# Performance work log

Measured on AMD Instinct MI355X. Metric: run time of the kernel, lower is better.

The kernel has to match this reference:

```python
import jax, jax.numpy as jnp
import numpy as np

B, T, D = 4, 4096, 1024

def setup_inputs() -> dict:
    key = jax.random.key(0)
    kx, kq, kk, kv = jax.random.split(key, 4)
    return {
        "x": jax.random.normal(kx, (B, T, D), dtype=jnp.float32),
        "w_q": jax.random.normal(kq, (D, D), dtype=jnp.float32),
        "w_k": jax.random.normal(kk, (D, D), dtype=jnp.float32),
        "w_v": jax.random.normal(kv, (D, D), dtype=jnp.float32),
    }

def reference(x, w_q, w_k, w_v):
    # Projections: (B,T,D) @ (D,D) -> (B,T,D)
    q = jnp.einsum('btk,kd->btd', x, w_q)
    k = jnp.einsum('btk,kd->btd', x, w_k)
    v = jnp.einsum('btk,kd->btd', x, w_v)
    d = x.shape[-1]
    # Faithful to source: gamma = 1/sqrt(1/d) = sqrt(d) (multiplies, not divides)
    gamma = jnp.sqrt(jnp.asarray(d, dtype=x.dtype))
    a = jnp.einsum('bqd,bkd->bqk', q, k) * gamma  # (B,T,T), no softmax
    y = jnp.einsum('bqt,btd->bqd', a, v)          # (B,T,D)
    return y
```

## Files before the change

### kernel.cpp

```cpp
#include <hip/hip_runtime.h>
#include <hip/hip_bf16.h>


typedef __attribute__((ext_vector_type(8))) short bf16x8;
typedef __attribute__((ext_vector_type(4))) float f32x4;

__device__ __forceinline__ unsigned short bf16bits(float f) {
    union { __hip_bfloat16 b; unsigned short s; } r;
    r.b = __float2bfloat16(f);
    return r.s;
}

__device__ __forceinline__ void gload16(const void* g, void* l) {
    __builtin_amdgcn_global_load_lds((__attribute__((address_space(1))) void*)g,
                                     (__attribute__((address_space(3))) void*)l,
                                     16, 0, 0);
}

template<int TM, int TN, bool OUT_F32>
__global__ __launch_bounds__(256)
void gemm_nt(const __hip_bfloat16* __restrict__ Ap, const __hip_bfloat16* __restrict__ Bp,
             void* __restrict__ Cp, int N, int Kc, int ldA, int ldB,
             long sA, long sB, long sC, int nb, float scale)
{
    constexpr int FM = TM / 32;
    constexpr int FN = TN / 32;

    __shared__ __hip_bfloat16 At[TM][32];
    __shared__ __hip_bfloat16 Bt[TN][32];

    const int bz    = blockIdx.z;
    const int batch = bz % nb;
    const int kc    = bz / nb;

    int wg = blockIdx.y * gridDim.x + blockIdx.x;
    const int cpx = (int)(gridDim.x * gridDim.y) >> 3;
    wg = (wg & 7) * cpx + (wg >> 3);
    const int n0 = (wg % (int)gridDim.x) * TN;
    const int m0 = (wg / (int)gridDim.x) * TM;

    const int tid  = threadIdx.x;
    const int lane = tid & 63;
    const int wave = tid >> 6;
    const int wm = (wave & 1) * (TM / 2);
    const int wn = (wave >> 1) * (TN / 2);
    const int l16 = lane & 15;
    const int lq  = lane >> 4;

    const int aoff = wave * (TM * 8) + lane * 8;
    const int boff = wave * (TN * 8) + lane * 8;

    const __hip_bfloat16* Ab = Ap + (size_t)batch * sA + (size_t)kc * Kc;
    const __hip_bfloat16* Bb = Bp + (size_t)batch * sB + (size_t)kc * Kc;

    f32x4 acc[FM][FN];
    #pragma unroll
    for (int i = 0; i < FM; ++i)
        #pragma unroll
        for (int j = 0; j < FN; ++j)
            acc[i][j] = (f32x4){0.f, 0.f, 0.f, 0.f};

    for (int k0 = 0; k0 < Kc; k0 += 32) {
        #pragma unroll
        for (int i = 0; i < TM / 64; ++i) {
            const __hip_bfloat16* s =
                Ab + (size_t)(m0 + (aoff >> 5) + i * 16) * ldA + k0 + (aoff & 31);
            gload16(s, (__hip_bfloat16*)At + aoff + i * 512);
        }
        #pragma unroll
        for (int i = 0; i < TN / 64; ++i) {
            const __hip_bfloat16* s =
                Bb + (size_t)(n0 + (boff >> 5) + i * 16) * ldB + k0 + (boff & 31);
            gload16(s, (__hip_bfloat16*)Bt + boff + i * 512);
        }
        __syncthreads();

        bf16x8 av[FM], bv[FN];
        #pragma unroll
        for (int i = 0; i < FM; ++i)
            av[i] = *(const bf16x8*)&At[wm + i * 16 + l16][lq * 8];
        #pragma unroll
        for (int j = 0; j < FN; ++j)
            bv[j] = *(const bf16x8*)&Bt[wn + j * 16 + l16][lq * 8];
        #pragma unroll
        for (int i = 0; i < FM; ++i)
            #pragma unroll
            for (int j = 0; j < FN; ++j)
                acc[i][j] = __builtin_amdgcn_mfma_f32_16x16x32_bf16(av[i], bv[j], acc[i][j], 0, 0, 0);
        __syncthreads();
    }

    float* Cf = (float*)Cp;
    __hip_bfloat16* Ch = (__hip_bfloat16*)Cp;
    const size_t cb0 = (size_t)bz * sC;
    #pragma unroll
    for (int i = 0; i < FM; ++i) {
        #pragma unroll
        for (int j = 0; j < FN; ++j) {
            const int row0 = m0 + wm + i * 16 + lq * 4;
            const int col  = n0 + wn + j * 16 + l16;
            #pragma unroll
            for (int r = 0; r < 4; ++r) {
                float v = acc[i][j][r] * scale;
                size_t idx = cb0 + (size_t)(row0 + r) * N + col;
                if (OUT_F32) Cf[idx] = v;
                else         Ch[idx] = __float2bfloat16(v);
            }
        }
    }
}

__global__ __launch_bounds__(256)
void reduce_kchunks(const unsigned short* __restrict__ part,
                    unsigned short* __restrict__ out)
{
    const size_t l = ((size_t)blockIdx.x * 256 + threadIdx.x) * 8;
    const size_t DD4 = (size_t)4 << 20;
    union { unsigned short h[8]; uint4 u; } a, b, o;
    a.u = *(const uint4*)(part + l);
    b.u = *(const uint4*)(part + l + DD4);
    #pragma unroll
    for (int j = 0; j < 8; ++j) {
        union { float f; unsigned int u; } fa, fb;
        fa.u = (unsigned int)a.h[j] << 16;
        fb.u = (unsigned int)b.h[j] << 16;
        o.h[j] = bf16bits(fa.f + fb.f);
    }
    *(uint4*)(out + l) = o.u;
}

#define TP 64
__global__ __launch_bounds__(256)
void transpose_cast(const float* __restrict__ in, __hip_bfloat16* __restrict__ out,
                    __hip_bfloat16* __restrict__ straight, int nsb,
                    int R, int C, long inStride, long outStride)
{
    __shared__ __hip_bfloat16 t2[TP][TP + 4];
    const int b  = blockIdx.z;
    const int r0 = blockIdx.x * TP;
    const int c0 = blockIdx.y * TP;
    const float* inb = in + (size_t)b * inStride;
    __hip_bfloat16* outb = out + (size_t)b * outStride;
    __hip_bfloat16* stb  = straight + (size_t)b * inStride;
    const int t  = threadIdx.x;
    const int rr = t >> 4;
    const int c4 = (t & 15) * 4;
    #pragma unroll
    for (int p = 0; p < 4; ++p) {
        const int row = p * 16 + rr;
        float4 f = *(const float4*)&inb[(size_t)(r0 + row) * C + c0 + c4];
        union { __hip_bfloat16 h[4]; uint2 u; } s;
        s.h[0] = __float2bfloat16(f.x); s.h[1] = __float2bfloat16(f.y);
        s.h[2] = __float2bfloat16(f.z); s.h[3] = __float2bfloat16(f.w);
        t2[c4 + 0][row] = s.h[0];
        t2[c4 + 1][row] = s.h[1];
        t2[c4 + 2][row] = s.h[2];
        t2[c4 + 3][row] = s.h[3];
        if (b < nsb)
            *(uint2*)&stb[(size_t)(r0 + row) * C + c0 + c4] = s.u;
    }
    __syncthreads();
    #pragma unroll
    for (int p = 0; p < 4; ++p) {
        const int crow = p * 16 + rr;
        union { __hip_bfloat16 h[4]; uint2 u; } o;
        #pragma unroll
        for (int j = 0; j < 4; ++j) o.h[j] = t2[crow][c4 + j];
        *(uint2*)&outb[(size_t)(c0 + crow) * R + r0 + c4] = o.u;
    }
}

__global__ __launch_bounds__(256)
void cast_f32_bf16(const float* __restrict__ in, __hip_bfloat16* __restrict__ out, int n)
{
    const int i = (blockIdx.x * 256 + threadIdx.x) << 2;
    if (i >= n) return;
    float4 f = *(const float4*)(in + i);
    union { __hip_bfloat16 h[4]; uint2 u; } t;
    t.h[0] = __float2bfloat16(f.x); t.h[1] = __float2bfloat16(f.y);
    t.h[2] = __float2bfloat16(f.z); t.h[3] = __float2bfloat16(f.w);
    *(uint2*)(out + i) = t.u;
}

extern "C" void kernel_launch(void* const* d_in, const int* in_sizes, int n_in,
                              void* d_out, int out_size, void* d_ws, size_t ws_size,
                              hipStream_t stream)
{
    const int Bz = 4, T = 4096, D = 1024;
    const float gamma = 32.0f;

    const float* x  = (const float*)d_in[0];
    const float* wq = (const float*)d_in[1];
    const float* wk = (const float*)d_in[2];
    const float* wv = (const float*)d_in[3];
    float* y = (float*)d_out;

    unsigned char* p = (unsigned char*)d_ws;
    const size_t DD = (size_t)D * D;
    __hip_bfloat16* Gb  = (__hip_bfloat16*)p; p += Bz * DD * 2;
    __hip_bfloat16* Hb  = (__hip_bfloat16*)p; p += Bz * DD * 2;
    __hip_bfloat16* PTb = (__hip_bfloat16*)p; p += Bz * DD * 2;
    __hip_bfloat16* wqb = (__hip_bfloat16*)p; p += DD * 2;
    __hip_bfloat16* wkb = (__hip_bfloat16*)p; p += DD * 2;
    __hip_bfloat16* wvT = (__hip_bfloat16*)p; p += DD * 2;
    __hip_bfloat16* C0b = (__hip_bfloat16*)p; p += DD * 2;
    __hip_bfloat16* Gpart = Hb;
    __hip_bfloat16* xb23  = Gb;

    __hip_bfloat16* xbT  = (__hip_bfloat16*)d_out;
    __hip_bfloat16* xb01 = (__hip_bfloat16*)((unsigned char*)d_out + ((size_t)32 << 20));

    dim3 blk(256);

    cast_f32_bf16<<<dim3((int)(DD / 1024)), blk, 0, stream>>>(wq, wqb, (int)DD);
    cast_f32_bf16<<<dim3((int)(DD / 1024)), blk, 0, stream>>>(wk, wkb, (int)DD);
    transpose_cast<<<dim3(D / TP, D / TP, 1), blk, 0, stream>>>(
        wv, wvT, wvT, 0, D, D, 0, 0);
    transpose_cast<<<dim3(T / TP, D / TP, Bz), blk, 0, stream>>>(
        x, xbT, xb01, 2, T, D, (long)T * D, (long)D * T);

    gemm_nt<64, 128, false><<<dim3(D / 128, D / 64, 1), blk, 0, stream>>>(
        wqb, wkb, C0b, D, D, D, D, 0, 0, 0, 1, 1.0f);
    gemm_nt<128, 128, false><<<dim3(D / 128, D / 128, 2 * Bz), blk, 0, stream>>>(
        xbT, xbT, Gpart, D, T / 2, T, T, (long)D * T, (long)D * T, (long)DD, Bz, 1.0f);
    reduce_kchunks<<<dim3((int)(Bz * DD / 2048)), blk, 0, stream>>>(
        (const unsigned short*)Gpart, (unsigned short*)Gb);
    gemm_nt<64, 128, false><<<dim3(D / 128, D / 64, Bz), blk, 0, stream>>>(
        C0b, Gb, Hb, D, D, D, D, 0, (long)DD, (long)DD, Bz, 1.0f);
    gemm_nt<64, 128, false><<<dim3(D / 128, D / 64, Bz), blk, 0, stream>>>(
        wvT, Hb, PTb, D, D, D, D, 0, (long)DD, (long)DD, Bz, gamma);

    cast_f32_bf16<<<dim3((int)(2 * (size_t)T * D / 1024)), blk, 0, stream>>>(
        x + (size_t)2 * T * D, xb23, (int)(2 * (size_t)T * D));

    gemm_nt<128, 128, true><<<dim3(D / 128, T / 128, 2), blk, 0, stream>>>(
        xb01, PTb, y, D, D, D, D, (long)T * D, (long)DD, (long)T * D, 2, 1.0f);
    gemm_nt<128, 128, true><<<dim3(D / 128, T / 128, 2), blk, 0, stream>>>(
        xb23, PTb + 2 * DD, y + (size_t)2 * T * D, D, D, D, D,
        (long)T * D, (long)DD, (long)T * D, 2, 1.0f);
}
```

Measured before the change: 326.1 us.

## Double-buffer GEMM LDS tiles and remap workgroups across XCDs per slice

The GEMM kernel now keeps two LDS buffers. The next K-tile is loaded asynchronously with global_load_lds while MFMAs run on the current tile, which leaves one barrier per iteration instead of two. It also adds template modes that remap the flat workgroup id so each XCD (id & 7) handles particular batch or k-chunk slices. This is meant to improve L2 locality for the batched GEMMs. The cost is twice the LDS per block, which may lower occupancy, and correctness relies on the barrier waiting for outstanding async loads.

```diff
diff --git a/kernel.cpp b/kernel.cpp
--- a/kernel.cpp
+++ b/kernel.cpp
@@ -17,7 +17,7 @@
                                      16, 0, 0);
 }
 
-template<int TM, int TN, bool OUT_F32>
+template<int TM, int TN, int MODE, bool OUT_F32>
 __global__ __launch_bounds__(256)
 void gemm_nt(const __hip_bfloat16* __restrict__ Ap, const __hip_bfloat16* __restrict__ Bp,
              void* __restrict__ Cp, int N, int Kc, int ldA, int ldB,
@@ -26,18 +26,32 @@
     constexpr int FM = TM / 32;
     constexpr int FN = TN / 32;
 
-    __shared__ __hip_bfloat16 At[TM][32];
-    __shared__ __hip_bfloat16 Bt[TN][32];
-
-    const int bz    = blockIdx.z;
-    const int batch = bz % nb;
-    const int kc    = bz / nb;
-
-    int wg = blockIdx.y * gridDim.x + blockIdx.x;
-    const int cpx = (int)(gridDim.x * gridDim.y) >> 3;
-    wg = (wg & 7) * cpx + (wg >> 3);
-    const int n0 = (wg % (int)gridDim.x) * TN;
-    const int m0 = (wg / (int)gridDim.x) * TM;
+    __shared__ __hip_bfloat16 At[2][TM][32];
+    __shared__ __hip_bfloat16 Bt[2][TN][32];
+
+    const int gx = (int)gridDim.x, gy = (int)gridDim.y, gz = (int)gridDim.z;
+    int slice, tile;
+    if (MODE == 0) {
+        slice = blockIdx.z;
+        int wg = blockIdx.y * gx + blockIdx.x;
+        const int cpx = (gx * gy) >> 3;
+        tile = (wg & 7) * cpx + (wg >> 3);
+    } else {
+        const int h = ((int)blockIdx.z * gy + (int)blockIdx.y) * gx + (int)blockIdx.x;
+        const int xcd = h & 7, k = h >> 3;
+        if (MODE == 1) {
+            const int SL = gz >> 3;
+            slice = xcd + 8 * (k % SL);
+            tile  = k / SL;
+        } else {
+            slice = xcd % gz;
+            tile  = (xcd / gz) * ((gx * gy * gz) >> 3) + k;
+        }
+    }
+    const int batch = slice % nb;
+    const int kc    = slice / nb;
+    const int n0 = (tile % gx) * TN;
+    const int m0 = (tile / gx) * TM;
 
     const int tid  = threadIdx.x;
     const int lane = tid & 63;
@@ -49,10 +63,23 @@
 
     const int aoff = wave * (TM * 8) + lane * 8;
     const int boff = wave * (TN * 8) + lane * 8;
+    const int arow = aoff >> 5, acol = aoff & 31;
+    const int brow = boff >> 5, bcol = boff & 31;
 
     const __hip_bfloat16* Ab = Ap + (size_t)batch * sA + (size_t)kc * Kc;
     const __hip_bfloat16* Bb = Bp + (size_t)batch * sB + (size_t)kc * Kc;
 
+    auto stage = [&](int buf, int k0) {
+        #pragma unroll
+        for (int i = 0; i < TM / 64; ++i)
+            gload16(Ab + (size_t)(m0 + arow + i * 16) * ldA + k0 + acol,
+                    &At[buf][0][0] + aoff + i * 512);
+        #pragma unroll
+        for (int i = 0; i < TN / 64; ++i)
+            gload16(Bb + (size_t)(n0 + brow + i * 16) * ldB + k0 + bcol,
+                    &Bt[buf][0][0] + boff + i * 512);
+    };
+
     f32x4 acc[FM][FN];
     #pragma unroll
     for (int i = 0; i < FM; ++i)
@@ -60,28 +87,21 @@
         for (int j = 0; j < FN; ++j)
             acc[i][j] = (f32x4){0.f, 0.f, 0.f, 0.f};
 
-    for (int k0 = 0; k0 < Kc; k0 += 32) {
-        #pragma unroll
-        for (int i = 0; i < TM / 64; ++i) {
-            const __hip_bfloat16* s =
-                Ab + (size_t)(m0 + (aoff >> 5) + i * 16) * ldA + k0 + (aoff & 31);
-            gload16(s, (__hip_bfloat16*)At + aoff + i * 512);
-        }
-        #pragma unroll
-        for (int i = 0; i < TN / 64; ++i) {
-            const __hip_bfloat16* s =
-                Bb + (size_t)(n0 + (boff >> 5) + i * 16) * ldB + k0 + (boff & 31);
-            gload16(s, (__hip_bfloat16*)Bt + boff + i * 512);
-        }
-        __syncthreads();
+    stage(0, 0);
+    __syncthreads();
+
+    const int nt = Kc >> 5;
+    for (int t = 0; t < nt; ++t) {
+        const int cur = t & 1;
+        if (t + 1 < nt) stage(cur ^ 1, (t + 1) << 5);
 
         bf16x8 av[FM], bv[FN];
         #pragma unroll
         for (int i = 0; i < FM; ++i)
-            av[i] = *(const bf16x8*)&At[wm + i * 16 + l16][lq * 8];
+            av[i] = *(const bf16x8*)&At[cur][wm + i * 16 + l16][lq * 8];
         #pragma unroll
         for (int j = 0; j < FN; ++j)
-            bv[j] = *(const bf16x8*)&Bt[wn + j * 16 + l16][lq * 8];
+            bv[j] = *(const bf16x8*)&Bt[cur][wn + j * 16 + l16][lq * 8];
         #pragma unroll
         for (int i = 0; i < FM; ++i)
             #pragma unroll
@@ -92,7 +112,7 @@
 
     float* Cf = (float*)Cp;
     __hip_bfloat16* Ch = (__hip_bfloat16*)Cp;
-    const size_t cb0 = (size_t)bz * sC;
+    const size_t cb0 = (size_t)slice * sC;
     #pragma unroll
     for (int i = 0; i < FM; ++i) {
         #pragma unroll
@@ -219,23 +239,23 @@
     transpose_cast<<<dim3(T / TP, D / TP, Bz), blk, 0, stream>>>(
         x, xbT, xb01, 2, T, D, (long)T * D, (long)D * T);
 
-    gemm_nt<64, 128, false><<<dim3(D / 128, D / 64, 1), blk, 0, stream>>>(
+    gemm_nt<64, 128, 0, false><<<dim3(D / 128, D / 64, 1), blk, 0, stream>>>(
         wqb, wkb, C0b, D, D, D, D, 0, 0, 0, 1, 1.0f);
-    gemm_nt<128, 128, false><<<dim3(D / 128, D / 128, 2 * Bz), blk, 0, stream>>>(
+    gemm_nt<128, 128, 1, false><<<dim3(D / 128, D / 128, 2 * Bz), blk, 0, stream>>>(
         xbT, xbT, Gpart, D, T / 2, T, T, (long)D * T, (long)D * T, (long)DD, Bz, 1.0f);
     reduce_kchunks<<<dim3((int)(Bz * DD / 2048)), blk, 0, stream>>>(
         (const unsigned short*)Gpart, (unsigned short*)Gb);
-    gemm_nt<64, 128, false><<<dim3(D / 128, D / 64, Bz), blk, 0, stream>>>(
+    gemm_nt<64, 128, 2, false><<<dim3(D / 128, D / 64, Bz), blk, 0, stream>>>(
         C0b, Gb, Hb, D, D, D, D, 0, (long)DD, (long)DD, Bz, 1.0f);
-    gemm_nt<64, 128, false><<<dim3(D / 128, D / 64, Bz), blk, 0, stream>>>(
+    gemm_nt<64, 128, 2, false><<<dim3(D / 128, D / 64, Bz), blk, 0, stream>>>(
         wvT, Hb, PTb, D, D, D, D, 0, (long)DD, (long)DD, Bz, gamma);
 
     cast_f32_bf16<<<dim3((int)(2 * (size_t)T * D / 1024)), blk, 0, stream>>>(
         x + (size_t)2 * T * D, xb23, (int)(2 * (size_t)T * D));
 
-    gemm_nt<128, 128, true><<<dim3(D / 128, T / 128, 2), blk, 0, stream>>>(
+    gemm_nt<128, 128, 2, true><<<dim3(D / 128, T / 128, 2), blk, 0, stream>>>(
         xb01, PTb, y, D, D, D, D, (long)T * D, (long)DD, (long)T * D, 2, 1.0f);
-    gemm_nt<128, 128, true><<<dim3(D / 128, T / 128, 2), blk, 0, stream>>>(
+    gemm_nt<128, 128, 2, true><<<dim3(D / 128, T / 128, 2), blk, 0, stream>>>(
         xb23, PTb + 2 * DD, y + (size_t)2 * T * D, D, D, D, D,
         (long)T * D, (long)DD, (long)T * D, 2, 1.0f);
 }
```

Result: faster. 297.3 us (-8.8%).
